# Optimization experiments

Measured on AMD Instinct MI355X. Metric: run time of the kernel, lower is better.

Reference implementation:

```python
import jax, jax.numpy as jnp
import numpy as np

B, S, H, NH = 2, 2048, 512, 8
DK = H // NH


def setup_inputs() -> dict:
    key = jax.random.key(0)
    ks = jax.random.split(key, 12)
    inp = {
        "query": jax.random.normal(ks[0], (B, S, H), dtype=jnp.float32),
        "key": jax.random.normal(ks[1], (B, S, H), dtype=jnp.float32),
        "value": jax.random.normal(ks[2], (B, S, H), dtype=jnp.float32),
        "bias": jax.random.normal(ks[3], (B, 1, S, S), dtype=jnp.float32),
        "mask": jax.random.randint(ks[4], (B, S), 0, 2, dtype=jnp.int32),
        "Wq": jax.random.normal(ks[5], (H, H), dtype=jnp.float32) * 0.02,
        "bq": jax.random.normal(ks[6], (H,), dtype=jnp.float32) * 0.02,
        "Wk": jax.random.normal(ks[7], (H, H), dtype=jnp.float32) * 0.02,
        "bk": jax.random.normal(ks[8], (H,), dtype=jnp.float32) * 0.02,
        "Wv": jax.random.normal(ks[9], (H, H), dtype=jnp.float32) * 0.02,
        "bv": jax.random.normal(ks[10], (H,), dtype=jnp.float32) * 0.02,
    }
    return inp


def reference(query, key, value, bias, mask, Wq, bq, Wk, bk, Wv, bv):
    b = query.shape[0]
    # torch nn.Linear: x @ W.T + b, then split heads -> [B, h, S, d_k]
    def proj(x, W, bb):
        y = x @ W.T + bb
        return y.reshape(b, -1, NH, DK).transpose(0, 2, 1, 3)

    q = proj(query, Wq, bq)
    k = proj(key, Wk, bk)
    v = proj(value, Wv, bv)

    score = jnp.einsum("bhqd,bhkd->bhqk", q, k) / np.sqrt(DK).astype(np.float32)
    # NOTE: the source swaps bias/mask when calling attention():
    #   the 0/1 mask is ADDED to the scores...
    mask_add = mask.reshape(b, 1, 1, -1).astype(score.dtype)
    score = score + mask_add
    #   ...and the float bias is used for the masked_fill (bias == 0 -> -1e30).
    score = jnp.where(bias == 0, jnp.asarray(-1e30, score.dtype), score)
    attn = jax.nn.softmax(score, axis=-1)  # dropout=None in the source call
    x = jnp.einsum("bhqk,bhkd->bhqd", attn, v)
    return x.transpose(0, 2, 1, 3).reshape(b, -1, NH * DK)
```

## Files before the change

kernel.cpp:

```cpp
#include <hip/hip_runtime.h>
#include <hip/hip_bf16.h>
#include <stdint.h>

#define B_  2
#define S_  2048
#define H_  512
#define NH_ 8
#define DK_ 64

typedef __bf16 bf16x8 __attribute__((ext_vector_type(8)));
typedef short  s16x4  __attribute__((ext_vector_type(4)));
typedef float  f32x4  __attribute__((ext_vector_type(4)));

static __device__ __forceinline__ uint32_t pk2(float a, float b) {
  __hip_bfloat162 h = __float22bfloat162_rn(float2{a, b});
  uint32_t u;
  __builtin_memcpy(&u, &h, 4);
  return u;
}

static __device__ __forceinline__ f32x4 mfma_k16(s16x4 a, s16x4 b, f32x4 c) {
#if defined(__HIP_DEVICE_COMPILE__)
  return __builtin_amdgcn_mfma_f32_16x16x16bf16_1k(a, b, c, 0, 0, 0);
#else
  (void)a; (void)b;
  return c;
#endif
}

typedef const __attribute__((address_space(1))) uint32_t* gas_t;
typedef __attribute__((address_space(3))) uint32_t* las_t;
static __device__ __forceinline__ void cp16(const void* g, void* l) {
  __builtin_amdgcn_global_load_lds((gas_t)g, (las_t)l, 16, 0, 0);
}

struct ProjArgs {
  const float* X[3];
  const float* W[3];
  const float* Bv[3];
  uint16_t*    O[3];
  const float* bias;
  const int*   mask;
  uint32_t*    zrow;
  float*       fmL;
};

__global__ __launch_bounds__(256) void prep_proj_kernel(ProjArgs pa) {
  __shared__ __align__(16) char psm[24640];
  int bid = blockIdx.x, t = threadIdx.x;

  if (bid >= 768) {
    if (bid < 1280) {
      int rr = bid - 768;
      const float* base = pa.bias + (size_t)rr * 8 * 2048 + t * 8;
      uint4 a[8], b2[8];
#pragma unroll
      for (int i = 0; i < 8; i++) {
        const uint4* src = (const uint4*)(base + (size_t)i * 2048);
        a[i] = src[0]; b2[i] = src[1];
      }
      uint32_t (*wbuf)[4] = (uint32_t (*)[4])psm;
      int wv = t >> 6, ln = t & 63;
#pragma unroll
      for (int i = 0; i < 8; i++) {
        bool z = ((a[i].x << 1) == 0u) | ((a[i].y << 1) == 0u) |
                 ((a[i].z << 1) == 0u) | ((a[i].w << 1) == 0u) |
                 ((b2[i].x << 1) == 0u) | ((b2[i].y << 1) == 0u) |
                 ((b2[i].z << 1) == 0u) | ((b2[i].w << 1) == 0u);
        uint64_t m = __ballot(z);
        if (ln == 0) {
          uint32_t bits = 0;
#pragma unroll
          for (int c = 0; c < 8; c++)
            bits |= (uint32_t)(((m >> (8 * c)) & 0xFFull) != 0ull) << c;
          wbuf[i][wv] = bits;
        }
      }
      __syncthreads();
      if (t < 8)
        pa.zrow[rr * 8 + t] = wbuf[t][0] | (wbuf[t][1] << 8) |
                              (wbuf[t][2] << 16) | (wbuf[t][3] << 24);
    } else {
      const float LOG2E = 1.44269504088896340736f;
#pragma unroll
      for (int i = 0; i < 16; i++) {
        int idx = i * 256 + t;
        pa.fmL[idx] = (float)pa.mask[idx] * LOG2E;
      }
    }
    return;
  }

  int xcd = bid & 7, j = bid >> 3;
  int gi = ((j >> 3) << 3) | xcd;
  int dtile = j & 7;
  int mat = gi >> 5, mtile = gi & 31;
  int m0 = mtile * 128, n0 = dtile * 64;
  const float* X  = pa.X[mat];
  const float* Wt = pa.W[mat];
  const float* Bv = pa.Bv[mat];
  uint16_t*    O  = pa.O[mat];

  uint16_t (*Xs)[64] = (uint16_t (*)[64])psm;
  uint16_t (*Ws)[64] = (uint16_t (*)[64])(psm + 16384);

  int w = t >> 6, l = t & 63, lo = l & 15, g = l >> 4;
  int lr = l >> 4;
  int lc = l & 15;

  const float* Xp = X + (size_t)(m0 + w * 32 + lr) * 512 + lc * 4;
  const float* Wp = Wt + (size_t)(n0 + w * 16 + lr) * 512 + lc * 4;

  f32x4 acc[2][4];
#pragma unroll
  for (int st = 0; st < 2; st++)
#pragma unroll
    for (int dt = 0; dt < 4; dt++) acc[st][dt] = (f32x4){0.f, 0.f, 0.f, 0.f};

  float4 xa[8], wa2[4];
#pragma unroll
  for (int i = 0; i < 8; i++) xa[i] = *(const float4*)(Xp + (size_t)i * 4 * 512);
#pragma unroll
  for (int i = 0; i < 4; i++) wa2[i] = *(const float4*)(Wp + (size_t)i * 4 * 512);

  for (int kb = 0; kb < 8; kb++) {
#pragma unroll
    for (int i = 0; i < 8; i++) {
      int r = w * 32 + i * 4 + lr;
      int s0 = (lc >> 1) ^ (r & 7);
      uint2 pk{pk2(xa[i].x, xa[i].y), pk2(xa[i].z, xa[i].w)};
      *(uint2*)&Xs[r][s0 * 8 + (lc & 1) * 4] = pk;
    }
#pragma unroll
    for (int i = 0; i < 4; i++) {
      int r = w * 16 + i * 4 + lr;
      int s0 = (lc >> 1) ^ (r & 7);
      uint2 pk{pk2(wa2[i].x, wa2[i].y), pk2(wa2[i].z, wa2[i].w)};
      *(uint2*)&Ws[r][s0 * 8 + (lc & 1) * 4] = pk;
    }
    __syncthreads();
    if (kb < 7) {
      const float* Xn = Xp + (kb + 1) * 64;
      const float* Wn = Wp + (kb + 1) * 64;
#pragma unroll
      for (int i = 0; i < 8; i++) xa[i] = *(const float4*)(Xn + (size_t)i * 4 * 512);
#pragma unroll
      for (int i = 0; i < 4; i++) wa2[i] = *(const float4*)(Wn + (size_t)i * 4 * 512);
    }
#pragma unroll
    for (int kk = 0; kk < 2; kk++) {
      int seg = (kk * 4 + g) ^ (lo & 7);
      bf16x8 xf[2], wf[4];
#pragma unroll
      for (int st = 0; st < 2; st++)
        xf[st] = *(const bf16x8*)&Xs[w * 32 + st * 16 + lo][seg * 8];
#pragma unroll
      for (int dt = 0; dt < 4; dt++)
        wf[dt] = *(const bf16x8*)&Ws[dt * 16 + lo][seg * 8];
      if (mat < 2) {
#pragma unroll
        for (int st = 0; st < 2; st++)
#pragma unroll
          for (int dt = 0; dt < 4; dt++)
            acc[st][dt] = __builtin_amdgcn_mfma_f32_16x16x32_bf16(wf[dt], xf[st], acc[st][dt], 0, 0, 0);
      } else {
#pragma unroll
        for (int st = 0; st < 2; st++)
#pragma unroll
          for (int dt = 0; dt < 4; dt++)
            acc[st][dt] = __builtin_amdgcn_mfma_f32_16x16x32_bf16(xf[st], wf[dt], acc[st][dt], 0, 0, 0);
      }
    }
    __syncthreads();
  }

  if (mat < 2) {
    float scale = (mat == 0) ? 0.125f : 1.0f;
    float4 bv4[4];
#pragma unroll
    for (int dt = 0; dt < 4; dt++)
      bv4[dt] = *(const float4*)(Bv + n0 + dt * 16 + g * 4);
#pragma unroll
    for (int st = 0; st < 2; st++) {
      int ss = m0 + w * 32 + st * 16 + lo;
      int bb = ss >> 11, sIn = ss & 2047;
      uint16_t* obase = O + ((size_t)(bb * NH_ + dtile) * S_ + sIn) * DK_;
#pragma unroll
      for (int dt = 0; dt < 4; dt++) {
        float v0 = (acc[st][dt][0] + bv4[dt].x) * scale;
        float v1 = (acc[st][dt][1] + bv4[dt].y) * scale;
        float v2 = (acc[st][dt][2] + bv4[dt].z) * scale;
        float v3 = (acc[st][dt][3] + bv4[dt].w) * scale;
        uint2 pk{pk2(v0, v1), pk2(v2, v3)};
        *(uint2*)(obase + dt * 16 + g * 4) = pk;
      }
    }
  } else {
    float bval[4];
#pragma unroll
    for (int dt = 0; dt < 4; dt++) bval[dt] = Bv[n0 + dt * 16 + lo];
#pragma unroll
    for (int st = 0; st < 2; st++) {
      int m = m0 + w * 32 + st * 16 + g * 4;
      int bb = m >> 11, sIn = m & 2047;
#pragma unroll
      for (int dt = 0; dt < 4; dt++) {
        int dd = dt * 16 + lo;
        float v0 = acc[st][dt][0] + bval[dt];
        float v1 = acc[st][dt][1] + bval[dt];
        float v2 = acc[st][dt][2] + bval[dt];
        float v3 = acc[st][dt][3] + bval[dt];
        uint2 pk{pk2(v0, v1), pk2(v2, v3)};
        *(uint2*)(O + ((size_t)(bb * NH_ + dtile) * DK_ + dd) * S_ + sIn) = pk;
      }
    }
  }
}

__global__ __launch_bounds__(256) void attn_kernel(
    const uint16_t* __restrict__ Qb, const uint16_t* __restrict__ Kb,
    const uint16_t* __restrict__ Vt, const uint32_t* __restrict__ zrow,
    const float* __restrict__ fmL, const float* __restrict__ bias,
    float* __restrict__ out) {
  int bid = blockIdx.x;
  int bh = bid & 15, qtile = bid >> 4;
  int b = bh >> 3, h = bh & 7;
  int q0 = qtile * 32;
  int t = threadIdx.x;
  int w = t >> 6, l = t & 63, lo = l & 15, g = l >> 4;

  __shared__ __align__(16) char smem[32768];
  uint16_t* KsB = (uint16_t*)smem;
  uint16_t* VsB = (uint16_t*)(smem + 16384);

  const uint16_t* Qh = Qb + (size_t)bh * S_ * DK_;
  const uint16_t* Kh = Kb + (size_t)bh * S_ * DK_;
  const uint16_t* Vh = Vt + (size_t)bh * DK_ * S_;

  int lrow = l >> 3, lseg = (l & 7) ^ lrow;
  const uint16_t* kbase = Kh + (size_t)(w * 16 + lrow) * DK_ + lseg * 8;
  const uint16_t* vbase = Vh + (size_t)(w * 16 + lrow) * S_ + lseg * 8;
  uint16_t* kd0 = KsB + (w * 16) * 64;
  uint16_t* kd8 = KsB + (w * 16 + 8) * 64;
  uint16_t* vd0 = VsB + (w * 16) * 64;
  uint16_t* vd8 = VsB + (w * 16 + 8) * 64;

  uint32_t zall = zrow[(b << 11) + q0 + (l & 31)];
#pragma unroll
  for (int s = 1; s < 32; s <<= 1) zall |= __shfl_xor(zall, s);

  bf16x8 qf[2][2];
#pragma unroll
  for (int qt = 0; qt < 2; qt++)
#pragma unroll
    for (int kk = 0; kk < 2; kk++)
      qf[qt][kk] = *(const bf16x8*)(Qh + (size_t)(q0 + qt * 16 + lo) * DK_ + kk * 32 + g * 8);

  f32x4 o[4][2];
#pragma unroll
  for (int dt = 0; dt < 4; dt++)
#pragma unroll
    for (int qt = 0; qt < 2; qt++) o[dt][qt] = (f32x4){0.f, 0.f, 0.f, 0.f};
  float ts[2] = {0.f, 0.f};

  const float* fmrow = fmL + b * S_ + w * 16 + g * 4;
  const float LOG2E = 1.44269504088896340736f;

  cp16(kbase, kd0);
  cp16(kbase + 512, kd8);
  cp16(vbase, vd0);
  cp16(vbase + 8 * S_, vd8);
  float4 mvc = *(const float4*)(fmrow);
  float4 mvn = mvc;

  for (int kb = 0; kb < 32; kb++) {
    int cur = kb & 1;
    int k0 = kb * 64;
    asm volatile("s_waitcnt vmcnt(0)" ::: "memory");
    __builtin_amdgcn_s_barrier();
    if (kb + 1 < 32) {
      int kn = k0 + 64;
      int nb = (cur ^ 1) * 4096;
      cp16(kbase + (size_t)kn * 64, kd0 + nb);
      cp16(kbase + (size_t)kn * 64 + 512, kd8 + nb);
      cp16(vbase + kn, vd0 + nb);
      cp16(vbase + kn + 8 * S_, vd8 + nb);
      mvn = *(const float4*)(fmrow + kn);
    }
    __builtin_amdgcn_sched_barrier(0);

    const uint16_t* KsT = KsB + cur * 4096;
    const uint16_t* VsT = VsB + cur * 4096;

    s16x4 vf[4];
    {
      int s = (2 * w + (g >> 1)) ^ (lo & 7);
      int off = s * 8 + (g & 1) * 4;
#pragma unroll
      for (int dt = 0; dt < 4; dt++)
        vf[dt] = *(const s16x4*)(VsT + (dt * 16 + lo) * 64 + off);
    }
    bf16x8 kf[2];
#pragma unroll
    for (int kk = 0; kk < 2; kk++) {
      int s = (kk * 4 + g) ^ (lo & 7);
      kf[kk] = *(const bf16x8*)(KsT + (w * 16 + lo) * 64 + s * 8);
    }

    f32x4 c[2];
#pragma unroll
    for (int qt = 0; qt < 2; qt++) {
      f32x4 z = {0.f, 0.f, 0.f, 0.f};
      z = __builtin_amdgcn_mfma_f32_16x16x32_bf16(kf[0], qf[qt][0], z, 0, 0, 0);
      c[qt] = __builtin_amdgcn_mfma_f32_16x16x32_bf16(kf[1], qf[qt][1], z, 0, 0, 0);
    }

    float4 mv4 = mvc;
    float p[2][4];
    if (((zall >> kb) & 1u) == 0u) {
#pragma unroll
      for (int qt = 0; qt < 2; qt++) {
        p[qt][0] = __builtin_amdgcn_exp2f(__builtin_fmaf(c[qt][0], LOG2E, mv4.x));
        p[qt][1] = __builtin_amdgcn_exp2f(__builtin_fmaf(c[qt][1], LOG2E, mv4.y));
        p[qt][2] = __builtin_amdgcn_exp2f(__builtin_fmaf(c[qt][2], LOG2E, mv4.z));
        p[qt][3] = __builtin_amdgcn_exp2f(__builtin_fmaf(c[qt][3], LOG2E, mv4.w));
      }
    } else {
#pragma unroll
      for (int qt = 0; qt < 2; qt++) {
        float4 bz = *(const float4*)(bias + ((size_t)(b * S_ + q0 + qt * 16 + lo)) * S_ + k0 + w * 16 + g * 4);
        p[qt][0] = (bz.x == 0.f) ? 0.f : __builtin_amdgcn_exp2f(__builtin_fmaf(c[qt][0], LOG2E, mv4.x));
        p[qt][1] = (bz.y == 0.f) ? 0.f : __builtin_amdgcn_exp2f(__builtin_fmaf(c[qt][1], LOG2E, mv4.y));
        p[qt][2] = (bz.z == 0.f) ? 0.f : __builtin_amdgcn_exp2f(__builtin_fmaf(c[qt][2], LOG2E, mv4.z));
        p[qt][3] = (bz.w == 0.f) ? 0.f : __builtin_amdgcn_exp2f(__builtin_fmaf(c[qt][3], LOG2E, mv4.w));
      }
    }

    s16x4 pf[2];
#pragma unroll
    for (int qt = 0; qt < 2; qt++) {
      ts[qt] += (p[qt][0] + p[qt][1]) + (p[qt][2] + p[qt][3]);
      union { s16x4 v; uint32_t u[2]; } uu;
      uu.u[0] = pk2(p[qt][0], p[qt][1]);
      uu.u[1] = pk2(p[qt][2], p[qt][3]);
      pf[qt] = uu.v;
    }

#pragma unroll
    for (int dt = 0; dt < 4; dt++)
#pragma unroll
      for (int qt = 0; qt < 2; qt++)
        o[dt][qt] = mfma_k16(vf[dt], pf[qt], o[dt][qt]);

    mvc = mvn;
  }

  float* OT = (float*)smem;
  float* LS = (float*)(smem + 8448);
#pragma unroll
  for (int qt = 0; qt < 2; qt++) {
    float v = ts[qt];
    v += __shfl_xor(v, 16);
    v += __shfl_xor(v, 32);
    ts[qt] = v;
  }
  __syncthreads();
  if (g == 0) {
#pragma unroll
    for (int qt = 0; qt < 2; qt++) LS[(w * 2 + qt) * 16 + lo] = ts[qt];
  }
#pragma unroll
  for (int ww = 0; ww < 4; ww++) {
    if (w == ww) {
#pragma unroll
      for (int dt = 0; dt < 4; dt++)
#pragma unroll
        for (int qt = 0; qt < 2; qt++)
#pragma unroll
          for (int r = 0; r < 4; r++) {
            int idx = (dt * 16 + g * 4 + r) * 33 + qt * 16 + lo;
            if (ww == 0) OT[idx] = o[dt][qt][r];
            else         OT[idx] += o[dt][qt][r];
          }
    }
    __syncthreads();
  }
  {
    int q = t >> 3, dseg = (t & 7) * 8;
    int qt2 = q >> 4, lo2 = q & 15;
    float lsum = LS[(0 * 2 + qt2) * 16 + lo2] + LS[(1 * 2 + qt2) * 16 + lo2] +
                 LS[(2 * 2 + qt2) * 16 + lo2] + LS[(3 * 2 + qt2) * 16 + lo2];
    float linv = 1.0f / fmaxf(lsum, 1e-30f);
    float* ob = out + ((size_t)(b * S_ + q0 + q)) * H_ + h * DK_ + dseg;
#pragma unroll
    for (int i = 0; i < 2; i++) {
      float4 v;
      v.x = OT[(dseg + i * 4 + 0) * 33 + q] * linv;
      v.y = OT[(dseg + i * 4 + 1) * 33 + q] * linv;
      v.z = OT[(dseg + i * 4 + 2) * 33 + q] * linv;
      v.w = OT[(dseg + i * 4 + 3) * 33 + q] * linv;
      *(float4*)(ob + i * 4) = v;
    }
  }
}

extern "C" void kernel_launch(void* const* d_in, const int* in_sizes, int n_in,
                              void* d_out, int out_size, void* d_ws, size_t ws_size,
                              hipStream_t stream) {
  const float* query = (const float*)d_in[0];
  const float* key   = (const float*)d_in[1];
  const float* value = (const float*)d_in[2];
  const float* bias  = (const float*)d_in[3];
  const int*   mask  = (const int*)d_in[4];
  const float* Wq = (const float*)d_in[5];
  const float* bq = (const float*)d_in[6];
  const float* Wk = (const float*)d_in[7];
  const float* bk = (const float*)d_in[8];
  const float* Wv = (const float*)d_in[9];
  const float* bv = (const float*)d_in[10];

  char* ws = (char*)d_ws;
  uint32_t* zrow = (uint32_t*)ws;
  float*    fmL  = (float*)(ws + 16384);
  uint16_t* Qb = (uint16_t*)(ws + (size_t)(1 << 20));
  uint16_t* Kb = (uint16_t*)(ws + (size_t)(5 << 20));
  uint16_t* Vt = (uint16_t*)(ws + (size_t)(9 << 20));

  ProjArgs pa;
  pa.X[0] = query; pa.X[1] = key; pa.X[2] = value;
  pa.W[0] = Wq;    pa.W[1] = Wk;  pa.W[2] = Wv;
  pa.Bv[0] = bq;   pa.Bv[1] = bk; pa.Bv[2] = bv;
  pa.O[0] = Qb;    pa.O[1] = Kb;  pa.O[2] = Vt;
  pa.bias = bias;  pa.mask = mask;
  pa.zrow = zrow;  pa.fmL = fmL;

  prep_proj_kernel<<<1281, 256, 0, stream>>>(pa);

  attn_kernel<<<1024, 256, 0, stream>>>(Qb, Kb, Vt, zrow, fmL, bias, (float*)d_out);
}
```

Before: 160.7 us.

## Double query tile per block to 64 rows to reuse K/V tiles

```diff
diff --git a/kernel.cpp b/kernel.cpp
--- a/kernel.cpp
+++ b/kernel.cpp
@@ -225,7 +225,7 @@
   int bid = blockIdx.x;
   int bh = bid & 15, qtile = bid >> 4;
   int b = bh >> 3, h = bh & 7;
-  int q0 = qtile * 32;
+  int q0 = qtile * 64;
   int t = threadIdx.x;
   int w = t >> 6, l = t & 63, lo = l & 15, g = l >> 4;
 
@@ -245,23 +245,23 @@
   uint16_t* vd0 = VsB + (w * 16) * 64;
   uint16_t* vd8 = VsB + (w * 16 + 8) * 64;
 
-  uint32_t zall = zrow[(b << 11) + q0 + (l & 31)];
-#pragma unroll
-  for (int s = 1; s < 32; s <<= 1) zall |= __shfl_xor(zall, s);
-
-  bf16x8 qf[2][2];
-#pragma unroll
-  for (int qt = 0; qt < 2; qt++)
+  uint32_t zall = zrow[(b << 11) + q0 + l];
+#pragma unroll
+  for (int s = 1; s < 64; s <<= 1) zall |= __shfl_xor(zall, s);
+
+  bf16x8 qf[4][2];
+#pragma unroll
+  for (int qt = 0; qt < 4; qt++)
 #pragma unroll
     for (int kk = 0; kk < 2; kk++)
       qf[qt][kk] = *(const bf16x8*)(Qh + (size_t)(q0 + qt * 16 + lo) * DK_ + kk * 32 + g * 8);
 
-  f32x4 o[4][2];
+  f32x4 o[4][4];
 #pragma unroll
   for (int dt = 0; dt < 4; dt++)
 #pragma unroll
-    for (int qt = 0; qt < 2; qt++) o[dt][qt] = (f32x4){0.f, 0.f, 0.f, 0.f};
-  float ts[2] = {0.f, 0.f};
+    for (int qt = 0; qt < 4; qt++) o[dt][qt] = (f32x4){0.f, 0.f, 0.f, 0.f};
+  float ts[4] = {0.f, 0.f, 0.f, 0.f};
 
   const float* fmrow = fmL + b * S_ + w * 16 + g * 4;
   const float LOG2E = 1.44269504088896340736f;
@@ -307,49 +307,49 @@
       kf[kk] = *(const bf16x8*)(KsT + (w * 16 + lo) * 64 + s * 8);
     }
 
-    f32x4 c[2];
-#pragma unroll
-    for (int qt = 0; qt < 2; qt++) {
+    f32x4 c[4];
+#pragma unroll
+    for (int qt = 0; qt < 4; qt++) {
       f32x4 z = {0.f, 0.f, 0.f, 0.f};
       z = __builtin_amdgcn_mfma_f32_16x16x32_bf16(kf[0], qf[qt][0], z, 0, 0, 0);
       c[qt] = __builtin_amdgcn_mfma_f32_16x16x32_bf16(kf[1], qf[qt][1], z, 0, 0, 0);
     }
 
     float4 mv4 = mvc;
-    float p[2][4];
+    s16x4 pf[4];
     if (((zall >> kb) & 1u) == 0u) {
 #pragma unroll
-      for (int qt = 0; qt < 2; qt++) {
-        p[qt][0] = __builtin_amdgcn_exp2f(__builtin_fmaf(c[qt][0], LOG2E, mv4.x));
-        p[qt][1] = __builtin_amdgcn_exp2f(__builtin_fmaf(c[qt][1], LOG2E, mv4.y));
-        p[qt][2] = __builtin_amdgcn_exp2f(__builtin_fmaf(c[qt][2], LOG2E, mv4.z));
-        p[qt][3] = __builtin_amdgcn_exp2f(__builtin_fmaf(c[qt][3], LOG2E, mv4.w));
+      for (int qt = 0; qt < 4; qt++) {
+        float p0 = __builtin_amdgcn_exp2f(__builtin_fmaf(c[qt][0], LOG2E, mv4.x));
+        float p1 = __builtin_amdgcn_exp2f(__builtin_fmaf(c[qt][1], LOG2E, mv4.y));
+        float p2 = __builtin_amdgcn_exp2f(__builtin_fmaf(c[qt][2], LOG2E, mv4.z));
+        float p3 = __builtin_amdgcn_exp2f(__builtin_fmaf(c[qt][3], LOG2E, mv4.w));
+        ts[qt] += (p0 + p1) + (p2 + p3);
+        union { s16x4 v; uint32_t u[2]; } uu;
+        uu.u[0] = pk2(p0, p1);
+        uu.u[1] = pk2(p2, p3);
+        pf[qt] = uu.v;
       }
     } else {
 #pragma unroll
-      for (int qt = 0; qt < 2; qt++) {
+      for (int qt = 0; qt < 4; qt++) {
         float4 bz = *(const float4*)(bias + ((size_t)(b * S_ + q0 + qt * 16 + lo)) * S_ + k0 + w * 16 + g * 4);
-        p[qt][0] = (bz.x == 0.f) ? 0.f : __builtin_amdgcn_exp2f(__builtin_fmaf(c[qt][0], LOG2E, mv4.x));
-        p[qt][1] = (bz.y == 0.f) ? 0.f : __builtin_amdgcn_exp2f(__builtin_fmaf(c[qt][1], LOG2E, mv4.y));
-        p[qt][2] = (bz.z == 0.f) ? 0.f : __builtin_amdgcn_exp2f(__builtin_fmaf(c[qt][2], LOG2E, mv4.z));
-        p[qt][3] = (bz.w == 0.f) ? 0.f : __builtin_amdgcn_exp2f(__builtin_fmaf(c[qt][3], LOG2E, mv4.w));
-      }
-    }
-
-    s16x4 pf[2];
-#pragma unroll
-    for (int qt = 0; qt < 2; qt++) {
-      ts[qt] += (p[qt][0] + p[qt][1]) + (p[qt][2] + p[qt][3]);
-      union { s16x4 v; uint32_t u[2]; } uu;
-      uu.u[0] = pk2(p[qt][0], p[qt][1]);
-      uu.u[1] = pk2(p[qt][2], p[qt][3]);
-      pf[qt] = uu.v;
+        float p0 = (bz.x == 0.f) ? 0.f : __builtin_amdgcn_exp2f(__builtin_fmaf(c[qt][0], LOG2E, mv4.x));
+        float p1 = (bz.y == 0.f) ? 0.f : __builtin_amdgcn_exp2f(__builtin_fmaf(c[qt][1], LOG2E, mv4.y));
+        float p2 = (bz.z == 0.f) ? 0.f : __builtin_amdgcn_exp2f(__builtin_fmaf(c[qt][2], LOG2E, mv4.z));
+        float p3 = (bz.w == 0.f) ? 0.f : __builtin_amdgcn_exp2f(__builtin_fmaf(c[qt][3], LOG2E, mv4.w));
+        ts[qt] += (p0 + p1) + (p2 + p3);
+        union { s16x4 v; uint32_t u[2]; } uu;
+        uu.u[0] = pk2(p0, p1);
+        uu.u[1] = pk2(p2, p3);
+        pf[qt] = uu.v;
+      }
     }
 
 #pragma unroll
     for (int dt = 0; dt < 4; dt++)
 #pragma unroll
-      for (int qt = 0; qt < 2; qt++)
+      for (int qt = 0; qt < 4; qt++)
         o[dt][qt] = mfma_k16(vf[dt], pf[qt], o[dt][qt]);
 
     mvc = mvn;
@@ -358,7 +358,7 @@
   float* OT = (float*)smem;
   float* LS = (float*)(smem + 8448);
 #pragma unroll
-  for (int qt = 0; qt < 2; qt++) {
+  for (int qt = 0; qt < 4; qt++) {
     float v = ts[qt];
     v += __shfl_xor(v, 16);
     v += __shfl_xor(v, 32);
@@ -367,40 +367,45 @@
   __syncthreads();
   if (g == 0) {
 #pragma unroll
-    for (int qt = 0; qt < 2; qt++) LS[(w * 2 + qt) * 16 + lo] = ts[qt];
-  }
-#pragma unroll
-  for (int ww = 0; ww < 4; ww++) {
-    if (w == ww) {
-#pragma unroll
-      for (int dt = 0; dt < 4; dt++)
-#pragma unroll
-        for (int qt = 0; qt < 2; qt++)
-#pragma unroll
-          for (int r = 0; r < 4; r++) {
-            int idx = (dt * 16 + g * 4 + r) * 33 + qt * 16 + lo;
-            if (ww == 0) OT[idx] = o[dt][qt][r];
-            else         OT[idx] += o[dt][qt][r];
-          }
+    for (int qt = 0; qt < 4; qt++) LS[(w * 4 + qt) * 16 + lo] = ts[qt];
+  }
+#pragma unroll
+  for (int qh = 0; qh < 2; qh++) {
+#pragma unroll
+    for (int ww = 0; ww < 4; ww++) {
+      if (w == ww) {
+#pragma unroll
+        for (int dt = 0; dt < 4; dt++)
+#pragma unroll
+          for (int qt = 0; qt < 2; qt++)
+#pragma unroll
+            for (int r = 0; r < 4; r++) {
+              int idx = (dt * 16 + g * 4 + r) * 33 + qt * 16 + lo;
+              float val = o[dt][qh * 2 + qt][r];
+              if (ww == 0) OT[idx] = val;
+              else         OT[idx] += val;
+            }
+      }
+      __syncthreads();
+    }
+    {
+      int q = t >> 3, dseg = (t & 7) * 8;
+      int qt2 = qh * 2 + (q >> 4), lo2 = q & 15;
+      float lsum = LS[(0 * 4 + qt2) * 16 + lo2] + LS[(1 * 4 + qt2) * 16 + lo2] +
+                   LS[(2 * 4 + qt2) * 16 + lo2] + LS[(3 * 4 + qt2) * 16 + lo2];
+      float linv = 1.0f / fmaxf(lsum, 1e-30f);
+      float* ob = out + ((size_t)(b * S_ + q0 + qh * 32 + q)) * H_ + h * DK_ + dseg;
+#pragma unroll
+      for (int i = 0; i < 2; i++) {
+        float4 v;
+        v.x = OT[(dseg + i * 4 + 0) * 33 + q] * linv;
+        v.y = OT[(dseg + i * 4 + 1) * 33 + q] * linv;
+        v.z = OT[(dseg + i * 4 + 2) * 33 + q] * linv;
+        v.w = OT[(dseg + i * 4 + 3) * 33 + q] * linv;
+        *(float4*)(ob + i * 4) = v;
+      }
     }
     __syncthreads();
-  }
-  {
-    int q = t >> 3, dseg = (t & 7) * 8;
-    int qt2 = q >> 4, lo2 = q & 15;
-    float lsum = LS[(0 * 2 + qt2) * 16 + lo2] + LS[(1 * 2 + qt2) * 16 + lo2] +
-                 LS[(2 * 2 + qt2) * 16 + lo2] + LS[(3 * 2 + qt2) * 16 + lo2];
-    float linv = 1.0f / fmaxf(lsum, 1e-30f);
-    float* ob = out + ((size_t)(b * S_ + q0 + q)) * H_ + h * DK_ + dseg;
-#pragma unroll
-    for (int i = 0; i < 2; i++) {
-      float4 v;
-      v.x = OT[(dseg + i * 4 + 0) * 33 + q] * linv;
-      v.y = OT[(dseg + i * 4 + 1) * 33 + q] * linv;
-      v.z = OT[(dseg + i * 4 + 2) * 33 + q] * linv;
-      v.w = OT[(dseg + i * 4 + 3) * 33 + q] * linv;
-      *(float4*)(ob + i * 4) = v;
-    }
   }
 }
 
@@ -436,5 +441,5 @@
 
   prep_proj_kernel<<<1281, 256, 0, stream>>>(pa);
 
-  attn_kernel<<<1024, 256, 0, stream>>>(Qb, Kb, Vt, zrow, fmL, bias, (float*)d_out);
-}
+  attn_kernel<<<512, 256, 0, stream>>>(Qb, Kb, Vt, zrow, fmL, bias, (float*)d_out);
+}
```

Result: no change. 159.3 us (-0.9%).
